# Performance work log

Measured on AMD Instinct MI355X. Metric: run time of the kernel, lower is better.

## Reference

```python
import jax, jax.numpy as jnp
import numpy as np

N, D_IN, FC_DIM, GROUP, NONGT, EMB = 4096, 12544, 1024, 16, 300, 64
DG = FC_DIM // GROUP  # 64 per-head dim


def extract_position_matrix(bbox, nongt_dim):
    xmin, ymin, xmax, ymax = jnp.split(bbox, 4, axis=1)  # each [N,1]
    bw = xmax - xmin + 1.0
    bh = ymax - ymin + 1.0
    cx = 0.5 * (xmin + xmax)
    cy = 0.5 * (ymin + ymax)
    dx = jnp.log(jnp.maximum(jnp.abs((cx - cx.T) / bw), 1e-3))
    dy = jnp.log(jnp.maximum(jnp.abs((cy - cy.T) / bh), 1e-3))
    dw = jnp.log(bw / bw.T)
    dh = jnp.log(bh / bh.T)
    # slice to first nongt_dim columns, stack -> [N, nongt, 4]
    return jnp.stack([dx[:, :nongt_dim], dy[:, :nongt_dim],
                      dw[:, :nongt_dim], dh[:, :nongt_dim]], axis=2)


def extract_position_embedding(pos_mat, feat_dim=64, wave_length=1000.0):
    n8 = feat_dim // 8
    feat_range = jnp.arange(n8, dtype=pos_mat.dtype)
    dim_mat = wave_length ** (8.0 / feat_dim * feat_range)  # [8]
    div = 100.0 * pos_mat[..., None] / dim_mat              # [N,nongt,4,8]
    emb = jnp.concatenate([jnp.sin(div), jnp.cos(div)], axis=3)  # [N,nongt,4,16]
    return emb.reshape(pos_mat.shape[0], pos_mat.shape[1], feat_dim)


def attention_multi_head(feat, pos_emb, Wpos, bpos, Wq, bq, Wk, bk, Wo, bo):
    # feat: [N, 1024], pos_emb: [N, nongt, 64]
    nongt_feat = feat[:NONGT]                                   # [nongt, 1024]
    aff_w = jax.nn.relu(pos_emb @ Wpos + bpos)                  # [N, nongt, G]
    aff_w = jnp.swapaxes(aff_w, 1, 2)                           # [N, G, nongt]
    q = (feat @ Wq + bq).reshape(-1, GROUP, DG)                 # [N, G, dg]
    k = (nongt_feat @ Wk + bk).reshape(NONGT, GROUP, DG)        # [nongt, G, dg]
    aff = jnp.einsum('ngd,mgd->ngm', q, k) * (1.0 / np.sqrt(DG))  # [N, G, nongt]
    logits = jnp.log(jnp.maximum(aff_w, 1e-6)) + aff
    p = jax.nn.softmax(logits, axis=2)                          # [N, G, nongt]
    out = jnp.einsum('ngm,mc->ngc', p, nongt_feat)              # [N, G, 1024]
    # grouped 1x1 conv: group g maps 1024 -> 64 outputs
    lin = jnp.einsum('ngc,goc->ngo', out, Wo) + bo.reshape(GROUP, DG)
    return lin.reshape(feat.shape[0], FC_DIM)


def setup_inputs() -> dict:
    key = jax.random.key(0)
    ks = jax.random.split(key, 20)
    roi_feat = jax.random.normal(ks[0], (N, D_IN), dtype=jnp.float32)
    u = jax.random.uniform(ks[1], (N, 4), dtype=jnp.float32)
    x1 = u[:, 0:1] * 500.0
    y1 = u[:, 1:2] * 500.0
    bbox = jnp.concatenate([x1, y1, x1 + u[:, 2:3] * 200.0 + 1.0,
                            y1 + u[:, 3:4] * 200.0 + 1.0], axis=1)
    def lin(k, fin, fout):
        s = 1.0 / np.sqrt(fin)
        return jax.random.normal(k, (fin, fout), dtype=jnp.float32) * s
    inp = {'roi_feat': roi_feat, 'bbox': bbox,
           'W_fc1': lin(ks[2], D_IN, FC_DIM), 'b_fc1': jnp.zeros((FC_DIM,), jnp.float32),
           'W_fc2': lin(ks[3], FC_DIM, FC_DIM), 'b_fc2': jnp.zeros((FC_DIM,), jnp.float32)}
    for i, base in [(1, 4), (2, 10)]:
        inp[f'Wpos{i}'] = lin(ks[base], EMB, GROUP)
        inp[f'bpos{i}'] = jnp.zeros((GROUP,), jnp.float32)
        inp[f'Wq{i}'] = lin(ks[base + 1], FC_DIM, FC_DIM)
        inp[f'bq{i}'] = jnp.zeros((FC_DIM,), jnp.float32)
        inp[f'Wk{i}'] = lin(ks[base + 2], FC_DIM, FC_DIM)
        inp[f'bk{i}'] = jnp.zeros((FC_DIM,), jnp.float32)
        inp[f'Wo{i}'] = jax.random.normal(ks[base + 3], (GROUP, DG, FC_DIM), dtype=jnp.float32) * (1.0 / np.sqrt(FC_DIM))
        inp[f'bo{i}'] = jnp.zeros((FC_DIM,), jnp.float32)
    return inp


def reference(roi_feat, bbox, W_fc1, b_fc1, W_fc2, b_fc2,
              Wpos1, bpos1, Wq1, bq1, Wk1, bk1, Wo1, bo1,
              Wpos2, bpos2, Wq2, bq2, Wk2, bk2, Wo2, bo2):
    pos_mat = extract_position_matrix(bbox, NONGT)
    pos_emb = extract_position_embedding(pos_mat, EMB)
    x = roi_feat
    for (Wf, bf, Wp, bp, Wq, bq, Wk, bk, Wo, bo) in [
        (W_fc1, b_fc1, Wpos1, bpos1, Wq1, bq1, Wk1, bk1, Wo1, bo1),
        (W_fc2, b_fc2, Wpos2, bpos2, Wq2, bq2, Wk2, bk2, Wo2, bo2)]:
        x = x @ Wf + bf
        attn = attention_multi_head(x, pos_emb, Wp, bp, Wq, bq, Wk, bk, Wo, bo)
        x = jax.nn.relu(x + attn)
    return x
```

## Files before the change

kernel.cpp:

```cpp
#include <hip/hip_runtime.h>


using bf16x8 = __attribute__((ext_vector_type(8))) short;
using u16x4  = __attribute__((ext_vector_type(4))) short;
using f32x4  = __attribute__((ext_vector_type(4))) float;
typedef unsigned short u16;
typedef unsigned int   u32;

#define DEV __device__ __forceinline__

DEV u16 f2bf(float f) {
  u32 u = __float_as_uint(f);
  return (u16)((u + 0x7FFFu + ((u >> 16) & 1u)) >> 16);
}
DEV float bf2f(u16 h) { return __uint_as_float(((u32)h) << 16); }

DEV f32x4 mfma16(bf16x8 a, bf16x8 b, f32x4 c) {
  return __builtin_amdgcn_mfma_f32_16x16x32_bf16(a, b, c, 0, 0, 0);
}
DEV void gload16(const u16* g, u16* l) {
  __builtin_amdgcn_global_load_lds((const __attribute__((address_space(1))) void*)g,
                                   (__attribute__((address_space(3))) void*)l, 16, 0, 0);
}

DEV void fsincos(float x, float* s, float* c) {
  float r = x * 0.15915494309189535f;
  r -= rintf(r);
  float a = r * 6.283185307179586f;
  *s = __sinf(a); *c = __cosf(a);
}

struct PrepArgs {
  const float* Wo1; u16* Wo1_b;
  const float* Wo2; u16* Wo2_b;
  const float* Wfc1; u16* Wfc1_t;
  const float* wsrc[5]; u16* wdst[5];
};

__global__ __launch_bounds__(256) void prep_kernel(PrepArgs p) {
  __shared__ float tp[32][36];
  int b = blockIdx.x, tid = threadIdx.x;
  if (b < 1024) {
    const float* src = (b < 512) ? p.Wo1 : p.Wo2;
    u16* dst = (b < 512) ? p.Wo1_b : p.Wo2_b;
    size_t i = ((size_t)(b & 511) * 256 + tid) * 8;
    float4 a = *(const float4*)(src + i);
    float4 c = *(const float4*)(src + i + 4);
    bf16x8 v;
    v[0]=(short)f2bf(a.x); v[1]=(short)f2bf(a.y); v[2]=(short)f2bf(a.z); v[3]=(short)f2bf(a.w);
    v[4]=(short)f2bf(c.x); v[5]=(short)f2bf(c.y); v[6]=(short)f2bf(c.z); v[7]=(short)f2bf(c.w);
    *(bf16x8*)(dst + i) = v;
    return;
  }
  const float* in; u16* out; int r0, c0, R, C;
  if (b < 13568) {
    int idx = b - 1024;
    in = p.Wfc1; out = p.Wfc1_t; R = 12544; C = 1024;
    r0 = (idx >> 5) * 32; c0 = (idx & 31) * 32;
  } else {
    int idx = b - 13568;
    int z = idx >> 10, rest = idx & 1023;
    in = p.wsrc[z]; out = p.wdst[z]; R = 1024; C = 1024;
    r0 = (rest >> 5) * 32; c0 = (rest & 31) * 32;
  }
  {
    int r = tid >> 3, c4 = (tid & 7) * 4;
    float4 v = *(const float4*)(in + (size_t)(r0 + r) * C + c0 + c4);
    *(float4*)&tp[r][c4] = v;
  }
  __syncthreads();
  {
    int c = tid >> 3, r4 = (tid & 7) * 4;
    u16x4 o;
    o[0] = (short)f2bf(tp[r4 + 0][c]); o[1] = (short)f2bf(tp[r4 + 1][c]);
    o[2] = (short)f2bf(tp[r4 + 2][c]); o[3] = (short)f2bf(tp[r4 + 3][c]);
    *(u16x4*)(out + (size_t)(c0 + c) * R + r0 + r4) = o;
  }
}

__global__ __launch_bounds__(512, 2) void gemm8p(
    const float* __restrict__ A, const u16* __restrict__ Bt,
    float* __restrict__ P) {
  const int K = 12544;
  __shared__ u16 lds[65536];
  int tid = threadIdx.x;
  int w = tid >> 6, l = tid & 63, h = l >> 4, l15 = l & 15;
  int wm = w >> 2, wn = w & 3;

  int b = ((blockIdx.x & 7) << 5) | (blockIdx.x >> 3);
  int bz = b >> 6, rest = b & 63;
  int bm = (rest & 15) * 256;
  int bn = (rest >> 4) * 256;
  size_t k0 = (size_t)bz * 3136;

  int arow = tid >> 3;
  int c0e = (tid & 7) * 4;
  const float* pA0 = A + (size_t)(bm + arow) * K + k0 + c0e;
  const float* pA1 = pA0 + 32;
  const size_t aseg = (size_t)64 * K;
  int awe0 = ((arow * 128 + c0e * 2) ^ ((arow & 7) << 4)) >> 1;
  int awe1 = ((arow * 128 + 64 + c0e * 2) ^ ((arow & 7) << 4)) >> 1;

  int X = ((tid >> 3) & 7) << 4;
  int lb2 = (tid * 16) ^ X;
  int lr = lb2 >> 7, lc = (lb2 & 127) >> 1;
  const u16* pB = Bt + (size_t)(bn + lr) * K + k0 + lc;
  const size_t o64 = (size_t)64 * K, o128 = (size_t)128 * K, o192 = (size_t)192 * K;

  int swz = (l15 & 7) << 3;
  int xk0 = (h * 8) ^ swz;
  int xk1 = 32 ^ xk0;
  int rA = (wm * 64 + l15) * 64;
  int rB = (wn * 32 + l15) * 64;

  f32x4 acc[8][4];
#pragma unroll
  for (int i = 0; i < 8; i++)
#pragma unroll
    for (int j = 0; j < 4; j++) acc[i][j] = (f32x4){0.f, 0.f, 0.f, 0.f};

  float4 a0[4], a1[4];
  bf16x8 af[4][2], bl[2][2], bh[2][2];

#define AISSUE(kk) { _Pragma("unroll") for (int s = 0; s < 4; s++) {     \
    a0[s] = *(const float4*)(pA0 + s * aseg + (kk));                     \
    a1[s] = *(const float4*)(pA1 + s * aseg + (kk)); } }
#define BISSUE(WB, kk) {                                                 \
    gload16(pB + (kk),        (WB) + tid * 8);                           \
    gload16(pB + o64 + (kk),  (WB) + 4096 + tid * 8);                    \
    gload16(pB + o128 + (kk), (WB) + 8192 + tid * 8);                    \
    gload16(pB + o192 + (kk), (WB) + 12288 + tid * 8); }
#define AWRITE(WA) { _Pragma("unroll") for (int s = 0; s < 4; s++) {     \
    u16x4 v0, v1;                                                        \
    v0[0]=(short)f2bf(a0[s].x); v0[1]=(short)f2bf(a0[s].y);              \
    v0[2]=(short)f2bf(a0[s].z); v0[3]=(short)f2bf(a0[s].w);              \
    v1[0]=(short)f2bf(a1[s].x); v1[1]=(short)f2bf(a1[s].y);              \
    v1[2]=(short)f2bf(a1[s].z); v1[3]=(short)f2bf(a1[s].w);              \
    *(u16x4*)&(WA)[awe0 + s * 4096] = v0;                                \
    *(u16x4*)&(WA)[awe1 + s * 4096] = v1; } }
#define READ_AF(BASE)                                                    \
  _Pragma("unroll") for (int i = 0; i < 4; i++) {                        \
    af[i][0] = *(const bf16x8*)&LA[(BASE) + rA + i * 1024 + xk0];        \
    af[i][1] = *(const bf16x8*)&LA[(BASE) + rA + i * 1024 + xk1];        \
  }
#define Q_MFMA(QR, QC, BF)                                               \
  __builtin_amdgcn_s_setprio(1);                                         \
  _Pragma("unroll") for (int i = 0; i < 4; i++)                          \
    _Pragma("unroll") for (int j = 0; j < 2; j++) {                      \
      acc[(QR)*4+i][(QC)*2+j] = mfma16(af[i][0], BF[j][0], acc[(QR)*4+i][(QC)*2+j]); \
      acc[(QR)*4+i][(QC)*2+j] = mfma16(af[i][1], BF[j][1], acc[(QR)*4+i][(QC)*2+j]); \
    }                                                                    \
  __builtin_amdgcn_s_setprio(0);

  AISSUE(0);
  BISSUE(lds + 16384, 0);
  AWRITE(lds);
  asm volatile("s_waitcnt vmcnt(0) lgkmcnt(0)" ::: "memory");
  __builtin_amdgcn_s_barrier();

  for (int t = 0; t < 49; t++) {
    const u16* LA = lds + (t & 1) * 32768;
    const u16* LB = LA + 16384;
    u16* WA = lds + ((t + 1) & 1) * 32768;
    u16* WB = WA + 16384;
    if (t < 48) {
      int ktn = (t + 1) * 64;
      AISSUE(ktn);
      BISSUE(WB, ktn);
    }
    __builtin_amdgcn_sched_barrier(0);
    READ_AF(0);
#pragma unroll
    for (int j = 0; j < 2; j++) {
      bl[j][0] = *(const bf16x8*)&LB[rB + j * 1024 + xk0];
      bl[j][1] = *(const bf16x8*)&LB[rB + j * 1024 + xk1];
    }
    Q_MFMA(0, 0, bl);
    __builtin_amdgcn_sched_barrier(0);
#pragma unroll
    for (int j = 0; j < 2; j++) {
      bh[j][0] = *(const bf16x8*)&LB[8192 + rB + j * 1024 + xk0];
      bh[j][1] = *(const bf16x8*)&LB[8192 + rB + j * 1024 + xk1];
    }
    Q_MFMA(0, 1, bh);
    __builtin_amdgcn_sched_barrier(0);
    READ_AF(8192);
    Q_MFMA(1, 1, bh);
    __builtin_amdgcn_sched_barrier(0);
    Q_MFMA(1, 0, bl);
    __builtin_amdgcn_sched_barrier(0);
    if (t < 48) { AWRITE(WA); }
    asm volatile("s_waitcnt vmcnt(0) lgkmcnt(0)" ::: "memory");
    __builtin_amdgcn_sched_barrier(0);
    __builtin_amdgcn_s_barrier();
  }
#undef AISSUE
#undef BISSUE
#undef AWRITE
#undef READ_AF
#undef Q_MFMA

  float* dst = P + (size_t)bz * 4096 * 1024;
#pragma unroll
  for (int qr = 0; qr < 2; qr++)
#pragma unroll
    for (int i = 0; i < 4; i++)
#pragma unroll
      for (int qc = 0; qc < 2; qc++)
#pragma unroll
        for (int j = 0; j < 2; j++) {
          int row0 = bm + qr * 128 + wm * 64 + i * 16 + h * 4;
          int col  = bn + qc * 128 + wn * 32 + j * 16 + l15;
          f32x4 v = acc[qr * 4 + i][qc * 2 + j];
#pragma unroll
          for (int r = 0; r < 4; r++)
            dst[(size_t)(row0 + r) * 1024 + col] = v[r];
        }
}

__constant__ float C100D[8] = {100.f, 42.16965034285822f, 17.78279410038923f,
                               7.498942093324559f, 3.1622776601683795f,
                               1.333521432163324f, 0.5623413251903491f,
                               0.23713737056616552f};

__global__ __launch_bounds__(256) void reduce_pos_kernel(
    const float* __restrict__ P, const float* __restrict__ bias,
    float* __restrict__ xf, u16* __restrict__ xb,
    const float* __restrict__ bbox,
    const float* __restrict__ Wpos1, const float* __restrict__ Wpos2,
    const float* __restrict__ bpos1, const float* __restrict__ bpos2,
    u16* __restrict__ logw1, u16* __restrict__ logw2) {
  __shared__ u16 pool[18944];
  int tid = threadIdx.x;
  if (blockIdx.x < 2048) {
    const size_t MN = (size_t)4096 * 1024;
    size_t i = ((size_t)blockIdx.x * 256 + tid) * 4;
    size_t stride = (size_t)2048 * 256 * 4;
    for (; i < MN; i += stride) {
      float4 a = *(const float4*)(P + i);
      float4 b = *(const float4*)(P + MN + i);
      float4 c = *(const float4*)(P + 2 * MN + i);
      float4 d = *(const float4*)(P + 3 * MN + i);
      float4 bv = *(const float4*)(bias + (i & 1023));
      float4 r;
      r.x = a.x + b.x + c.x + d.x + bv.x;
      r.y = a.y + b.y + c.y + d.y + bv.y;
      r.z = a.z + b.z + c.z + d.z + bv.z;
      r.w = a.w + b.w + c.w + d.w + bv.w;
      *(float4*)(xf + i) = r;
      u16x4 hv;
      hv[0] = (short)f2bf(r.x); hv[1] = (short)f2bf(r.y);
      hv[2] = (short)f2bf(r.z); hv[3] = (short)f2bf(r.w);
      *(u16x4*)(xb + i) = hv;
    }
    return;
  }
  u16* emb_s = pool;
  u16* wp_s  = pool + 5632;
  u16* lw_s  = pool + 8448;
  int n = blockIdx.x - 2048;
  int w = tid >> 6, l = tid & 63, h = l >> 4, l15 = l & 15;
  for (int idx = tid; idx < 1024; idx += 256) {
    int e = idx >> 4, c = idx & 15;
    wp_s[c * 88 + e]        = f2bf(Wpos1[idx]);
    wp_s[(16 + c) * 88 + e] = f2bf(Wpos2[idx]);
  }
  float4 bn = ((const float4*)bbox)[n];
  float bw_n = bn.z - bn.x + 1.f, bh_n = bn.w - bn.y + 1.f;
  float cx_n = 0.5f * (bn.x + bn.z), cy_n = 0.5f * (bn.y + bn.w);
  float bps0 = bpos1[l15], bps1 = bpos2[l15];
  int p = tid >> 2, k = tid & 3;

  for (int m0 = 0; m0 < 320; m0 += 64) {
    int m = m0 + p;
    float4 bm = ((const float4*)bbox)[m];
    float v;
    if (k == 0)      v = logf(fmaxf(fabsf((cx_n - 0.5f * (bm.x + bm.z)) / bw_n), 1e-3f));
    else if (k == 1) v = logf(fmaxf(fabsf((cy_n - 0.5f * (bm.y + bm.w)) / bh_n), 1e-3f));
    else if (k == 2) v = logf(bw_n / (bm.z - bm.x + 1.f));
    else             v = logf(bh_n / (bm.w - bm.y + 1.f));
    __syncthreads();
#pragma unroll
    for (int tt = 0; tt < 8; tt++) {
      float s, c; fsincos(v * C100D[tt], &s, &c);
      emb_s[p * 88 + k * 16 + tt]     = f2bf(s);
      emb_s[p * 88 + k * 16 + 8 + tt] = f2bf(c);
    }
    __syncthreads();
    f32x4 acc0 = {0.f, 0.f, 0.f, 0.f}, acc1 = {0.f, 0.f, 0.f, 0.f};
    bf16x8 a0 = *(const bf16x8*)&emb_s[(w * 16 + l15) * 88 + h * 8];
    bf16x8 a1 = *(const bf16x8*)&emb_s[(w * 16 + l15) * 88 + 32 + h * 8];
    bf16x8 b00 = *(const bf16x8*)&wp_s[l15 * 88 + h * 8];
    bf16x8 b01 = *(const bf16x8*)&wp_s[l15 * 88 + 32 + h * 8];
    bf16x8 b10 = *(const bf16x8*)&wp_s[(16 + l15) * 88 + h * 8];
    bf16x8 b11 = *(const bf16x8*)&wp_s[(16 + l15) * 88 + 32 + h * 8];
    acc0 = mfma16(a0, b00, acc0); acc0 = mfma16(a1, b01, acc0);
    acc1 = mfma16(a0, b10, acc1); acc1 = mfma16(a1, b11, acc1);
#pragma unroll
    for (int r = 0; r < 4; r++) {
      int mm = m0 + w * 16 + h * 4 + r;
      lw_s[l15 * 328 + mm]        = f2bf(logf(fmaxf(acc0[r] + bps0, 1e-6f)));
      lw_s[(16 + l15) * 328 + mm] = f2bf(logf(fmaxf(acc1[r] + bps1, 1e-6f)));
    }
  }
  __syncthreads();
  for (int i = tid; i < 1280; i += 256) {
    int layer = i / 640, rest = i - layer * 640;
    int gg = rest / 40, seg = rest - gg * 40;
    bf16x8 v = *(const bf16x8*)&lw_s[(layer * 16 + gg) * 328 + seg * 8];
    u16* dst = (layer ? logw2 : logw1) + ((size_t)gg * 4096 + n) * 320 + seg * 8;
    *(bf16x8*)dst = v;
  }
}

struct GDesc {
  const u16* A; const u16* Bt; const float* bias;
  u16* Cb; float* Cf;
  int M, N, K, ldc, nt;
};

__global__ __launch_bounds__(256, 2) void gemmU(GDesc g0, GDesc g1, GDesc g2,
                                                int c0, int c1) {
  __shared__ u16 lds[32768];
  GDesc g; int lb = blockIdx.x;
  if (lb < c0) { g = g0; lb = (lb & 7) * (c0 >> 3) + (lb >> 3); }
  else if (lb < c1) { g = g1; lb -= c0; }
  else { g = g2; lb -= c1; }
  int bm = (lb / g.nt) * 128, bn = (lb % g.nt) * 128;
  int tid = threadIdx.x;
  int w = tid >> 6, l = tid & 63, h = l >> 4, l15 = l & 15;
  int wm = w >> 1, wn = w & 1;
  int K = g.K;

  int X = ((tid >> 3) & 7) << 4;
  int lbyte = (tid * 16) ^ X;
  int lr = lbyte >> 7, lc = (lbyte & 127) >> 1;
  const u16 *pa[4], *pb[4];
#pragma unroll
  for (int c = 0; c < 4; c++) {
    pa[c] = g.A  + (size_t)min(bm + c * 32 + lr, g.M - 1) * K + lc;
    pb[c] = g.Bt + (size_t)min(bn + c * 32 + lr, g.N - 1) * K + lc;
  }

  int swz = (l15 & 7) << 3;
  int xk0 = (h * 8) ^ swz;
  int xk1 = 32 ^ xk0;
  int rA = (wm * 64 + l15) * 64;
  int rB = (wn * 64 + l15) * 64;

  f32x4 acc[4][4];
#pragma unroll
  for (int i = 0; i < 4; i++)
#pragma unroll
    for (int j = 0; j < 4; j++) acc[i][j] = (f32x4){0.f, 0.f, 0.f, 0.f};

#define ISSUEU(W, kk)                                     \
  { gload16(pa[0] + (kk), (W) + tid * 8);                 \
    gload16(pa[1] + (kk), (W) + 2048 + tid * 8);          \
    gload16(pa[2] + (kk), (W) + 4096 + tid * 8);          \
    gload16(pa[3] + (kk), (W) + 6144 + tid * 8);          \
    gload16(pb[0] + (kk), (W) + 8192 + tid * 8);          \
    gload16(pb[1] + (kk), (W) + 10240 + tid * 8);         \
    gload16(pb[2] + (kk), (W) + 12288 + tid * 8);         \
    gload16(pb[3] + (kk), (W) + 14336 + tid * 8); }

  ISSUEU(lds, 0);
  int ktiles = K >> 6;
  for (int t = 0; t < ktiles; t++) {
    const u16* LA = lds + (t & 1) * 16384;
    const u16* LB = LA + 8192;
    u16* W = lds + ((t ^ 1) & 1) * 16384;
    if (t < ktiles - 1) {
      ISSUEU(W, (t + 1) * 64);
      asm volatile("s_waitcnt vmcnt(8)" ::: "memory");
    } else {
      asm volatile("s_waitcnt vmcnt(0)" ::: "memory");
    }
    __builtin_amdgcn_s_barrier();
    asm volatile("" ::: "memory");
    bf16x8 a[4][2], bfr[4][2];
#pragma unroll
    for (int i = 0; i < 4; i++) {
      a[i][0] = *(const bf16x8*)&LA[rA + i * 1024 + xk0];
      a[i][1] = *(const bf16x8*)&LA[rA + i * 1024 + xk1];
    }
#pragma unroll
    for (int j = 0; j < 4; j++) {
      bfr[j][0] = *(const bf16x8*)&LB[rB + j * 1024 + xk0];
      bfr[j][1] = *(const bf16x8*)&LB[rB + j * 1024 + xk1];
    }
    __builtin_amdgcn_s_setprio(1);
#pragma unroll
    for (int i = 0; i < 4; i++)
#pragma unroll
      for (int j = 0; j < 4; j++) {
        acc[i][j] = mfma16(a[i][0], bfr[j][0], acc[i][j]);
        acc[i][j] = mfma16(a[i][1], bfr[j][1], acc[i][j]);
      }
    __builtin_amdgcn_s_setprio(0);
    asm volatile("" ::: "memory");
    __builtin_amdgcn_s_barrier();
  }
#undef ISSUEU

#pragma unroll
  for (int i = 0; i < 4; i++) {
#pragma unroll
    for (int j = 0; j < 4; j++) {
      int col = bn + wn * 64 + j * 16 + l15;
      if (col >= g.ldc) continue;
      float bv = (g.bias != nullptr && col < g.N) ? g.bias[col] : 0.f;
      int row0 = bm + wm * 64 + i * 16 + h * 4;
#pragma unroll
      for (int r = 0; r < 4; r++) {
        int row = row0 + r;
        if (row >= g.M) continue;
        float v = acc[i][j][r] + bv;
        size_t off = (size_t)row * g.ldc + col;
        g.Cb[off] = f2bf(v);
        if (g.Cf != nullptr) g.Cf[off] = v;
      }
    }
  }
}

template <bool LAST>
__global__ __launch_bounds__(256) void attn_kernel(
    const u16* __restrict__ qb, const u16* __restrict__ kb,
    const u16* __restrict__ kvt, const u16* __restrict__ logw,
    const float* __restrict__ xf, const float* __restrict__ bo,
    float* __restrict__ outf, u16* __restrict__ outb) {
  __shared__ u16 ps[64 * 344];
  int tid = threadIdx.x;
  int g = blockIdx.y, n0 = blockIdx.x * 64;
  int w = tid >> 6, l = tid & 63, h = l >> 4, l15 = l & 15;

  {
    const u16* src = logw + ((size_t)g * 4096 + n0) * 320;
    for (int i = tid; i < 64 * 40; i += 256) {
      int row = i / 40, seg = i - row * 40;
      *(bf16x8*)&ps[row * 328 + seg * 8] = *(const bf16x8*)(src + row * 320 + seg * 8);
    }
  }
  int nrow = n0 + w * 16 + l15;
  const u16* qp = qb + (size_t)nrow * 1024 + g * 64;
  bf16x8 aq0 = *(const bf16x8*)(qp + h * 8);
  bf16x8 aq1 = *(const bf16x8*)(qp + 32 + h * 8);

  f32x4 acc[19];
#pragma unroll
  for (int f = 0; f < 19; f++) acc[f] = (f32x4){0.f, 0.f, 0.f, 0.f};
  const u16* kp = kb + g * 64 + h * 8;
#pragma unroll
  for (int f = 0; f < 19; f++) {
    bf16x8 b0 = *(const bf16x8*)(kp + (size_t)(f * 16 + l15) * 1024);
    bf16x8 b1 = *(const bf16x8*)(kp + (size_t)(f * 16 + l15) * 1024 + 32);
    acc[f] = mfma16(aq0, b0, acc[f]);
    acc[f] = mfma16(aq1, b1, acc[f]);
  }
  __syncthreads();

  int nbase = n0 + w * 16 + h * 4;
  int lrow = w * 16 + h * 4;
  float mx[4] = {-INFINITY, -INFINITY, -INFINITY, -INFINITY};
  float sm[4] = {0.f, 0.f, 0.f, 0.f};
#pragma unroll
  for (int f = 0; f < 19; f++) {
    int m = f * 16 + l15;
#pragma unroll
    for (int r = 0; r < 4; r++) {
      float lw = -INFINITY;
      if (m < 300) lw = bf2f(ps[(lrow + r) * 328 + m]);
      float lg = acc[f][r] * 0.125f + lw;
      acc[f][r] = lg;
      mx[r] = fmaxf(mx[r], lg);
    }
  }
#pragma unroll
  for (int d = 1; d < 16; d <<= 1)
#pragma unroll
    for (int r = 0; r < 4; r++) mx[r] = fmaxf(mx[r], __shfl_xor(mx[r], d));
#pragma unroll
  for (int f = 0; f < 19; f++)
#pragma unroll
    for (int r = 0; r < 4; r++) {
      float p = __expf(acc[f][r] - mx[r]);
      acc[f][r] = p; sm[r] += p;
    }
#pragma unroll
  for (int d = 1; d < 16; d <<= 1)
#pragma unroll
    for (int r = 0; r < 4; r++) sm[r] += __shfl_xor(sm[r], d);
  float inv[4];
#pragma unroll
  for (int r = 0; r < 4; r++) inv[r] = 1.f / sm[r];

  __syncthreads();
#pragma unroll
  for (int f = 0; f < 19; f++)
#pragma unroll
    for (int r = 0; r < 4; r++)
      ps[(lrow + r) * 344 + f * 16 + l15] = f2bf(acc[f][r]);
#pragma unroll
  for (int r = 0; r < 4; r++)
    ps[(lrow + r) * 344 + 304 + l15] = 0;

  f32x4 acc2[4];
#pragma unroll
  for (int fo = 0; fo < 4; fo++) acc2[fo] = (f32x4){0.f, 0.f, 0.f, 0.f};
  const u16* vp = kvt + (size_t)g * 64 * 320 + h * 8;
#pragma unroll
  for (int ks = 0; ks < 10; ks++) {
    bf16x8 ap = *(const bf16x8*)&ps[(w * 16 + l15) * 344 + ks * 32 + h * 8];
#pragma unroll
    for (int fo = 0; fo < 4; fo++) {
      bf16x8 bv = *(const bf16x8*)(vp + (size_t)(fo * 16 + l15) * 320 + ks * 32);
      acc2[fo] = mfma16(ap, bv, acc2[fo]);
    }
  }
#pragma unroll
  for (int fo = 0; fo < 4; fo++) {
    int col = g * 64 + fo * 16 + l15;
    float bov = bo[col];
#pragma unroll
    for (int r = 0; r < 4; r++) {
      int row = nbase + r;
      float v = xf[(size_t)row * 1024 + col] + acc2[fo][r] * inv[r] + bov;
      v = fmaxf(v, 0.f);
      if (LAST) outf[(size_t)row * 1024 + col] = v;
      else      outb[(size_t)row * 1024 + col] = f2bf(v);
    }
  }
}

extern "C" void kernel_launch(void* const* d_in, const int* in_sizes, int n_in,
                              void* d_out, int out_size, void* d_ws, size_t ws_size,
                              hipStream_t stream) {
  (void)in_sizes; (void)n_in; (void)out_size; (void)ws_size;
  const float* roi   = (const float*)d_in[0];
  const float* bbox  = (const float*)d_in[1];
  const float* Wfc1  = (const float*)d_in[2];
  const float* bfc1  = (const float*)d_in[3];
  const float* Wfc2  = (const float*)d_in[4];
  const float* bfc2  = (const float*)d_in[5];
  const float* Wpos1 = (const float*)d_in[6];
  const float* bpos1 = (const float*)d_in[7];
  const float* Wq1   = (const float*)d_in[8];
  const float* bq1   = (const float*)d_in[9];
  const float* Wk1   = (const float*)d_in[10];
  const float* bk1   = (const float*)d_in[11];
  const float* Wo1   = (const float*)d_in[12];
  const float* bo1   = (const float*)d_in[13];
  const float* Wpos2 = (const float*)d_in[14];
  const float* bpos2 = (const float*)d_in[15];
  const float* Wq2   = (const float*)d_in[16];
  const float* bq2   = (const float*)d_in[17];
  const float* Wk2   = (const float*)d_in[18];
  const float* bk2   = (const float*)d_in[19];
  const float* Wo2   = (const float*)d_in[20];
  const float* bo2   = (const float*)d_in[21];

  char* ws = (char*)d_ws;
  u16*  Wfc1_t = (u16*)(ws + 102760448);
  u16*  Wfc2_t = (u16*)(ws + 128450560);
  u16*  Wq1_t  = (u16*)(ws + 130547712);
  u16*  Wk1_t  = (u16*)(ws + 132644864);
  u16*  Wq2_t  = (u16*)(ws + 134742016);
  u16*  Wk2_t  = (u16*)(ws + 136839168);
  u16*  Wo1_b  = (u16*)(ws + 138936320);
  u16*  Wo2_b  = (u16*)(ws + 141033472);
  float* Pp    = (float*)(ws + 143134720);
  float* xf    = (float*)(ws + 227020800);
  u16*  xb_f   = (u16*)(ws + 243798016);
  u16*  xb_a   = (u16*)(ws + 252186624);
  u16*  q_b    = (u16*)(ws + 260575232);
  u16*  k_b    = (u16*)(ws + 268963840);
  u16*  kvt_b  = (u16*)(ws + 269578240);
  u16*  logw1  = (u16*)(ws + 270233600);
  u16*  logw2  = (u16*)(ws + 312176640);

  {
    PrepArgs p;
    p.Wo1 = Wo1;   p.Wo1_b = Wo1_b;
    p.Wo2 = Wo2;   p.Wo2_b = Wo2_b;
    p.Wfc1 = Wfc1; p.Wfc1_t = Wfc1_t;
    p.wsrc[0] = Wfc2; p.wdst[0] = Wfc2_t;
    p.wsrc[1] = Wq1;  p.wdst[1] = Wq1_t;
    p.wsrc[2] = Wk1;  p.wdst[2] = Wk1_t;
    p.wsrc[3] = Wq2;  p.wdst[3] = Wq2_t;
    p.wsrc[4] = Wk2;  p.wdst[4] = Wk2_t;
    prep_kernel<<<18688, 256, 0, stream>>>(p);
  }
  gemm8p<<<256, 512, 0, stream>>>(roi, Wfc1_t, Pp);
  reduce_pos_kernel<<<6144, 256, 0, stream>>>(Pp, bfc1, xf, xb_f, bbox,
                                              Wpos1, Wpos2, bpos1, bpos2,
                                              logw1, logw2);
  {
    GDesc q  = {xb_f,  Wq1_t, bq1, q_b,   nullptr, 4096, 1024, 1024, 1024, 8};
    GDesc kk = {xb_f,  Wk1_t, bk1, k_b,   nullptr,  300, 1024, 1024, 1024, 8};
    GDesc kv = {Wo1_b, xb_f,  nullptr, kvt_b, nullptr, 1024, 300, 1024, 320, 3};
    gemmU<<<304, 256, 0, stream>>>(q, kk, kv, 256, 280);
  }
  attn_kernel<false><<<dim3(64, 16), 256, 0, stream>>>(q_b, k_b, kvt_b, logw1, xf, bo1, nullptr, xb_a);

  {
    GDesc fc = {xb_a, Wfc2_t, bfc2, xb_f, xf, 4096, 1024, 1024, 1024, 8};
    gemmU<<<256, 256, 0, stream>>>(fc, fc, fc, 256, 256);
  }
  {
    GDesc q  = {xb_f,  Wq2_t, bq2, q_b,   nullptr, 4096, 1024, 1024, 1024, 8};
    GDesc kk = {xb_f,  Wk2_t, bk2, k_b,   nullptr,  300, 1024, 1024, 1024, 8};
    GDesc kv = {Wo2_b, xb_f,  nullptr, kvt_b, nullptr, 1024, 300, 1024, 320, 3};
    gemmU<<<304, 256, 0, stream>>>(q, kk, kv, 256, 280);
  }
  attn_kernel<true><<<dim3(64, 16), 256, 0, stream>>>(q_b, k_b, kvt_b, logw2, xf, bo2, (float*)d_out, nullptr);
}
```

Measured before the change: 425.7 us.

## Split B prefetch into halves, interleave with MFMA, and widen A LDS writes

Restructures the main K-loop of the split-K fc1 GEMM. The B tile's global-to-LDS loads are now issued in two halves between MFMA quadrants, with partial vmcnt waits and barriers in place of one full drain at the end of each iteration, and the final iteration is peeled. The A tile load is also remapped so each thread converts 8 contiguous floats and does a single 16-byte LDS write instead of two 8-byte writes. The aim is to overlap memory latency with compute and cut LDS write instructions. The cost is an extra barrier per iteration, and the hand-counted vmcnt values make correctness depend on the exact order in which loads are issued.

```diff
diff --git a/kernel.cpp b/kernel.cpp
--- a/kernel.cpp
+++ b/kernel.cpp
@@ -94,12 +94,10 @@
   size_t k0 = (size_t)bz * 3136;
 
   int arow = tid >> 3;
-  int c0e = (tid & 7) * 4;
-  const float* pA0 = A + (size_t)(bm + arow) * K + k0 + c0e;
-  const float* pA1 = pA0 + 32;
+  int c0 = (tid & 7) * 8;
+  const float* pA0 = A + (size_t)(bm + arow) * K + k0 + c0;
   const size_t aseg = (size_t)64 * K;
-  int awe0 = ((arow * 128 + c0e * 2) ^ ((arow & 7) << 4)) >> 1;
-  int awe1 = ((arow * 128 + 64 + c0e * 2) ^ ((arow & 7) << 4)) >> 1;
+  int awe = ((arow * 128 + c0 * 2) ^ ((arow & 7) << 4)) >> 1;
 
   int X = ((tid >> 3) & 7) << 4;
   int lb2 = (tid * 16) ^ X;
@@ -124,25 +122,33 @@
 
 #define AISSUE(kk) { _Pragma("unroll") for (int s = 0; s < 4; s++) {     \
     a0[s] = *(const float4*)(pA0 + s * aseg + (kk));                     \
-    a1[s] = *(const float4*)(pA1 + s * aseg + (kk)); } }
-#define BISSUE(WB, kk) {                                                 \
+    a1[s] = *(const float4*)(pA0 + s * aseg + (kk) + 4); } }
+#define BISSUE_LO(WB, kk) {                                              \
     gload16(pB + (kk),        (WB) + tid * 8);                           \
-    gload16(pB + o64 + (kk),  (WB) + 4096 + tid * 8);                    \
+    gload16(pB + o64 + (kk),  (WB) + 4096 + tid * 8); }
+#define BISSUE_HI(WB, kk) {                                              \
     gload16(pB + o128 + (kk), (WB) + 8192 + tid * 8);                    \
     gload16(pB + o192 + (kk), (WB) + 12288 + tid * 8); }
 #define AWRITE(WA) { _Pragma("unroll") for (int s = 0; s < 4; s++) {     \
-    u16x4 v0, v1;                                                        \
-    v0[0]=(short)f2bf(a0[s].x); v0[1]=(short)f2bf(a0[s].y);              \
-    v0[2]=(short)f2bf(a0[s].z); v0[3]=(short)f2bf(a0[s].w);              \
-    v1[0]=(short)f2bf(a1[s].x); v1[1]=(short)f2bf(a1[s].y);              \
-    v1[2]=(short)f2bf(a1[s].z); v1[3]=(short)f2bf(a1[s].w);              \
-    *(u16x4*)&(WA)[awe0 + s * 4096] = v0;                                \
-    *(u16x4*)&(WA)[awe1 + s * 4096] = v1; } }
+    bf16x8 v;                                                            \
+    v[0]=(short)f2bf(a0[s].x); v[1]=(short)f2bf(a0[s].y);                \
+    v[2]=(short)f2bf(a0[s].z); v[3]=(short)f2bf(a0[s].w);                \
+    v[4]=(short)f2bf(a1[s].x); v[5]=(short)f2bf(a1[s].y);                \
+    v[6]=(short)f2bf(a1[s].z); v[7]=(short)f2bf(a1[s].w);                \
+    *(bf16x8*)&(WA)[awe + s * 4096] = v; } }
 #define READ_AF(BASE)                                                    \
   _Pragma("unroll") for (int i = 0; i < 4; i++) {                        \
     af[i][0] = *(const bf16x8*)&LA[(BASE) + rA + i * 1024 + xk0];        \
     af[i][1] = *(const bf16x8*)&LA[(BASE) + rA + i * 1024 + xk1];        \
   }
+#define READ_BL {                                                        \
+  _Pragma("unroll") for (int j = 0; j < 2; j++) {                        \
+    bl[j][0] = *(const bf16x8*)&LB[rB + j * 1024 + xk0];                 \
+    bl[j][1] = *(const bf16x8*)&LB[rB + j * 1024 + xk1]; } }
+#define READ_BH {                                                        \
+  _Pragma("unroll") for (int j = 0; j < 2; j++) {                        \
+    bh[j][0] = *(const bf16x8*)&LB[8192 + rB + j * 1024 + xk0];          \
+    bh[j][1] = *(const bf16x8*)&LB[8192 + rB + j * 1024 + xk1]; } }
 #define Q_MFMA(QR, QC, BF)                                               \
   __builtin_amdgcn_s_setprio(1);                                         \
   _Pragma("unroll") for (int i = 0; i < 4; i++)                          \
@@ -151,54 +157,73 @@
       acc[(QR)*4+i][(QC)*2+j] = mfma16(af[i][1], BF[j][1], acc[(QR)*4+i][(QC)*2+j]); \
     }                                                                    \
   __builtin_amdgcn_s_setprio(0);
+#define SBAR __builtin_amdgcn_sched_barrier(0)
 
   AISSUE(0);
-  BISSUE(lds + 16384, 0);
+  BISSUE_LO(lds + 16384, 0);
+  BISSUE_HI(lds + 16384, 0);
   AWRITE(lds);
   asm volatile("s_waitcnt vmcnt(0) lgkmcnt(0)" ::: "memory");
   __builtin_amdgcn_s_barrier();
 
-  for (int t = 0; t < 49; t++) {
+  for (int t = 0; t < 48; t++) {
     const u16* LA = lds + (t & 1) * 32768;
     const u16* LB = LA + 16384;
     u16* WA = lds + ((t + 1) & 1) * 32768;
     u16* WB = WA + 16384;
-    if (t < 48) {
-      int ktn = (t + 1) * 64;
-      AISSUE(ktn);
-      BISSUE(WB, ktn);
-    }
-    __builtin_amdgcn_sched_barrier(0);
+    int ktn = (t + 1) * 64;
+    AISSUE(ktn);
+    asm volatile("s_waitcnt vmcnt(10) lgkmcnt(0)" ::: "memory");
+    __builtin_amdgcn_s_barrier();
+    SBAR;
     READ_AF(0);
-#pragma unroll
-    for (int j = 0; j < 2; j++) {
-      bl[j][0] = *(const bf16x8*)&LB[rB + j * 1024 + xk0];
-      bl[j][1] = *(const bf16x8*)&LB[rB + j * 1024 + xk1];
-    }
+    READ_BL;
     Q_MFMA(0, 0, bl);
-    __builtin_amdgcn_sched_barrier(0);
-#pragma unroll
-    for (int j = 0; j < 2; j++) {
-      bh[j][0] = *(const bf16x8*)&LB[8192 + rB + j * 1024 + xk0];
-      bh[j][1] = *(const bf16x8*)&LB[8192 + rB + j * 1024 + xk1];
-    }
+    SBAR;
+    BISSUE_LO(WB, ktn);
+    asm volatile("s_waitcnt vmcnt(10)" ::: "memory");
+    __builtin_amdgcn_s_barrier();
+    SBAR;
+    READ_BH;
     Q_MFMA(0, 1, bh);
-    __builtin_amdgcn_sched_barrier(0);
+    SBAR;
+    BISSUE_HI(WB, ktn);
     READ_AF(8192);
     Q_MFMA(1, 1, bh);
-    __builtin_amdgcn_sched_barrier(0);
+    SBAR;
     Q_MFMA(1, 0, bl);
-    __builtin_amdgcn_sched_barrier(0);
-    if (t < 48) { AWRITE(WA); }
-    asm volatile("s_waitcnt vmcnt(0) lgkmcnt(0)" ::: "memory");
-    __builtin_amdgcn_sched_barrier(0);
+    SBAR;
+    AWRITE(WA);
+  }
+  {
+    const u16* LA = lds;
+    const u16* LB = lds + 16384;
+    asm volatile("s_waitcnt vmcnt(2) lgkmcnt(0)" ::: "memory");
     __builtin_amdgcn_s_barrier();
+    SBAR;
+    READ_AF(0);
+    READ_BL;
+    Q_MFMA(0, 0, bl);
+    SBAR;
+    asm volatile("s_waitcnt vmcnt(0)" ::: "memory");
+    __builtin_amdgcn_s_barrier();
+    SBAR;
+    READ_BH;
+    Q_MFMA(0, 1, bh);
+    SBAR;
+    READ_AF(8192);
+    Q_MFMA(1, 1, bh);
+    Q_MFMA(1, 0, bl);
   }
 #undef AISSUE
-#undef BISSUE
+#undef BISSUE_LO
+#undef BISSUE_HI
 #undef AWRITE
 #undef READ_AF
+#undef READ_BL
+#undef READ_BH
 #undef Q_MFMA
+#undef SBAR
 
   float* dst = P + (size_t)bz * 4096 * 1024;
 #pragma unroll
```

Result: faster. 409.6 us (-3.8%).
